# Performance work log

Hardware: AMD Instinct MI355X
Metric: run time of the kernel (lower is better)

The kernel has to match this reference:

```python
import jax, jax.numpy as jnp
import numpy as np

N_NODES = 50000
N_EDGES = 600000
IN_FEATS = 16
H_FEAT = 128
N_CLASSES = 4
N_HIDDEN_LAYERS = 19  # conv2..conv20


def setup_inputs() -> dict:
    key = jax.random.key(0)
    ks = jax.random.split(key, 10)
    x = jax.random.normal(ks[0], (N_NODES, IN_FEATS), dtype=jnp.float32)
    edge_index = jax.random.randint(ks[1], (2, N_EDGES), 0, N_NODES, dtype=jnp.int32)
    edge_attr = jax.random.uniform(ks[2], (N_EDGES, 1), dtype=jnp.float32)
    s_in = 1.0 / np.sqrt(IN_FEATS)
    s_h = 1.0 / np.sqrt(H_FEAT)
    W_in = jax.random.uniform(ks[3], (IN_FEATS, H_FEAT), minval=-s_in, maxval=s_in, dtype=jnp.float32)
    b_in = jax.random.uniform(ks[4], (H_FEAT,), minval=-s_in, maxval=s_in, dtype=jnp.float32)
    W_h = jax.random.uniform(ks[5], (N_HIDDEN_LAYERS, H_FEAT, H_FEAT), minval=-s_h, maxval=s_h, dtype=jnp.float32)
    b_h = jax.random.uniform(ks[6], (N_HIDDEN_LAYERS, H_FEAT), minval=-s_h, maxval=s_h, dtype=jnp.float32)
    W_fc = jax.random.uniform(ks[7], (H_FEAT, N_CLASSES), minval=-s_h, maxval=s_h, dtype=jnp.float32)
    b_fc = jax.random.uniform(ks[8], (N_CLASSES,), minval=-s_h, maxval=s_h, dtype=jnp.float32)
    return {"x": x, "edge_index": edge_index, "edge_attr": edge_attr,
            "W_in": W_in, "b_in": b_in, "W_h": W_h, "b_h": b_h,
            "W_fc": W_fc, "b_fc": b_fc}


def reference(x, edge_index, edge_attr, W_in, b_in, W_h, b_h, W_fc, b_fc):
    src, dst = edge_index[0], edge_index[1]
    ew = edge_attr[:, 0]  # edge_weight = edge_attr[:, 0]
    n = x.shape[0]
    # degree by dst, clamped at 1
    deg = jax.ops.segment_sum(jnp.ones(src.shape[0], dtype=x.dtype), dst, num_segments=n)
    deg_inv = 1.0 / jnp.maximum(deg, 1.0)  # [N]

    def conv(h, W, b):
        h = h @ W + b                       # [N, out]
        msg = h[src] * ew[:, None]          # [E, out]
        agg = jax.ops.segment_sum(msg, dst, num_segments=n)
        return agg * deg_inv[:, None]

    h = jax.nn.leaky_relu(conv(x, W_in, b_in))

    def step(h, params):
        W, b = params
        return jax.nn.leaky_relu(conv(h, W, b)), None

    h, _ = jax.lax.scan(step, h, (W_h, b_h))
    return h @ W_fc + b_fc  # [N, num_classes]
```

## Files before the change

### kernel.cpp

```cpp
#include <hip/hip_runtime.h>
#include <hip/hip_fp16.h>

#define N_NODES 50000
#define N_EDGES 600000
#define IN_F 16
#define HF 128
#define NC 4
#define NHL 19
#define N_FP8_LAYERS 15
#define WS_STRIDE 136

__device__ __forceinline__ float lrelu(float x) { return x > 0.f ? x : 0.01f * x; }

struct h4 { __half2 a, b; };

typedef _Float16 f16;
typedef _Float16 f16x8 __attribute__((ext_vector_type(8)));
typedef float    f32x4 __attribute__((ext_vector_type(4)));
typedef float    f32x2 __attribute__((ext_vector_type(2)));

__device__ __forceinline__ unsigned pack_fp8x4(float a, float b, float c, float d) {
    int r = __builtin_amdgcn_cvt_pk_fp8_f32(a, b, 0, false);
    r = __builtin_amdgcn_cvt_pk_fp8_f32(c, d, r, true);
    return (unsigned)r;
}


__global__ void count_deg_k(const int* __restrict__ dst, int* __restrict__ cnt) {
    int e = blockIdx.x * 256 + threadIdx.x;
    if (e < N_EDGES) atomicAdd(&cnt[dst[e]], 1);
}

__global__ void scan_k(const int* __restrict__ cnt, int* __restrict__ rowptr,
                       float* __restrict__ dinv) {
    __shared__ int wsum[16];
    __shared__ int carry_s;
    int t = threadIdx.x;
    int lane = t & 63, wid = t >> 6;
    if (t == 0) carry_s = 0;
    __syncthreads();
    for (int base = 0; base < N_NODES; base += 4096) {
        int idx = base + t * 4;
        int4 v = make_int4(0, 0, 0, 0);
        if (idx + 3 < N_NODES) v = *(const int4*)&cnt[idx];
        else {
            if (idx     < N_NODES) v.x = cnt[idx];
            if (idx + 1 < N_NODES) v.y = cnt[idx + 1];
            if (idx + 2 < N_NODES) v.z = cnt[idx + 2];
            if (idx + 3 < N_NODES) v.w = cnt[idx + 3];
        }
        if (idx + 3 < N_NODES) {
            float4 dv = make_float4(1.f / fmaxf((float)v.x, 1.f), 1.f / fmaxf((float)v.y, 1.f),
                                    1.f / fmaxf((float)v.z, 1.f), 1.f / fmaxf((float)v.w, 1.f));
            *(float4*)&dinv[idx] = dv;
        } else {
            if (idx     < N_NODES) dinv[idx]     = 1.f / fmaxf((float)v.x, 1.f);
            if (idx + 1 < N_NODES) dinv[idx + 1] = 1.f / fmaxf((float)v.y, 1.f);
            if (idx + 2 < N_NODES) dinv[idx + 2] = 1.f / fmaxf((float)v.z, 1.f);
            if (idx + 3 < N_NODES) dinv[idx + 3] = 1.f / fmaxf((float)v.w, 1.f);
        }
        int s1 = v.x + v.y, s2 = s1 + v.z, total = s2 + v.w;
        int sc = total;
#pragma unroll
        for (int off = 1; off < 64; off <<= 1) {
            int u = __shfl_up(sc, off, 64);
            if (lane >= off) sc += u;
        }
        if (lane == 63) wsum[wid] = sc;
        __syncthreads();
        if (t < 16) {
            int w = wsum[t];
#pragma unroll
            for (int off = 1; off < 16; off <<= 1) {
                int u = __shfl_up(w, off, 64);
                if (t >= off) w += u;
            }
            wsum[t] = w;
        }
        __syncthreads();
        int prefix = carry_s + (wid > 0 ? wsum[wid - 1] : 0) + (sc - total);
        if (idx     < N_NODES) rowptr[idx]     = prefix;
        if (idx + 1 < N_NODES) rowptr[idx + 1] = prefix + v.x;
        if (idx + 2 < N_NODES) rowptr[idx + 2] = prefix + s1;
        if (idx + 3 < N_NODES) rowptr[idx + 3] = prefix + s2;
        __syncthreads();
        if (t == 0) carry_s += wsum[15];
        __syncthreads();
    }
    if (t == 0) rowptr[N_NODES] = carry_s;
}

__global__ void fill_k(const int* __restrict__ src, const int* __restrict__ dst,
                       const float* __restrict__ ea, const int* __restrict__ rowptr,
                       int* __restrict__ fill, int2* __restrict__ edg,
                       const float* __restrict__ dinv) {
    int e = blockIdx.x * 256 + threadIdx.x;
    if (e < N_EDGES) {
        int d = dst[e];
        int pos = rowptr[d] + atomicAdd(&fill[d], 1);
        edg[pos] = make_int2(src[e], __float_as_int(ea[e] * dinv[d]));
    }
}


__global__ void wconv_k(const float* __restrict__ Wh, __half* __restrict__ Wt) {
    int idx = blockIdx.x * 256 + threadIdx.x;
    if (idx >= NHL * HF * HF) return;
    int l = idx / (HF * HF);
    int r = idx - l * (HF * HF);
    int n = r >> 7;
    int k = r & 127;
    Wt[idx] = __float2half(Wh[(size_t)l * HF * HF + k * HF + n]);
}


__global__ void gemm_in_k(const float* __restrict__ X, const float* __restrict__ W,
                          const float* __restrict__ b, unsigned* __restrict__ T8) {
    __shared__ float Ws[IN_F * HF];
    int t = threadIdx.x;
    ((float4*)Ws)[t]       = ((const float4*)W)[t];
    ((float4*)Ws)[t + 256] = ((const float4*)W)[t + 256];
    __syncthreads();
    int row = blockIdx.x * 16 + (t >> 4);
    if (row >= N_NODES) return;
    int tx = t & 15;
    int c0 = tx * 4, c1 = 64 + tx * 4;
    float4 a0 = *(const float4*)&b[c0];
    float4 a1 = *(const float4*)&b[c1];
    const float4* xr = (const float4*)(X + row * IN_F);
#pragma unroll
    for (int k4 = 0; k4 < 4; k4++) {
        float4 xv = xr[k4];
        const float* xp = (const float*)&xv;
#pragma unroll
        for (int kk = 0; kk < 4; kk++) {
            int k = k4 * 4 + kk;
            float4 w0 = *(const float4*)&Ws[k * HF + c0];
            float4 w1 = *(const float4*)&Ws[k * HF + c1];
            float xs = xp[kk];
            a0.x = fmaf(xs, w0.x, a0.x); a0.y = fmaf(xs, w0.y, a0.y);
            a0.z = fmaf(xs, w0.z, a0.z); a0.w = fmaf(xs, w0.w, a0.w);
            a1.x = fmaf(xs, w1.x, a1.x); a1.y = fmaf(xs, w1.y, a1.y);
            a1.z = fmaf(xs, w1.z, a1.z); a1.w = fmaf(xs, w1.w, a1.w);
        }
    }
    T8[(size_t)row * 32 + tx]      = pack_fp8x4(a0.x, a0.y, a0.z, a0.w);
    T8[(size_t)row * 32 + 16 + tx] = pack_fp8x4(a1.x, a1.y, a1.z, a1.w);
}


template <bool FP8IN, bool FP8OUT>
__global__ __launch_bounds__(256) void gemm_mfma_k(const void* __restrict__ Hin,
                                                   const __half* __restrict__ Wt,
                                                   const float* __restrict__ b,
                                                   void* __restrict__ Tout) {
    __shared__ __half Ws[HF * WS_STRIDE];
    __shared__ __half Hs[64 * WS_STRIDE];
    int t = threadIdx.x;
    int rbase = blockIdx.x * 64;
    int u16 = t & 15;
    int rg  = t >> 4;

#pragma unroll
    for (int p = 0; p < 8; p++) {
        int n = p * 16 + rg;
        *(float4*)&Ws[n * WS_STRIDE + u16 * 8] = *(const float4*)&Wt[(size_t)n * HF + u16 * 8];
    }
#pragma unroll
    for (int p = 0; p < 4; p++) {
        int rl = p * 16 + rg;
        int row = rbase + rl;
        if (row >= N_NODES) row = N_NODES - 1;
        if (FP8IN) {
            uint2 hv8 = *(const uint2*)&((const unsigned char*)Hin)[(size_t)row * HF + u16 * 8];
            f32x2 a0 = __builtin_amdgcn_cvt_pk_f32_fp8((int)hv8.x, false);
            f32x2 a1 = __builtin_amdgcn_cvt_pk_f32_fp8((int)hv8.x, true);
            f32x2 a2 = __builtin_amdgcn_cvt_pk_f32_fp8((int)hv8.y, false);
            f32x2 a3 = __builtin_amdgcn_cvt_pk_f32_fp8((int)hv8.y, true);
            h4 o0, o1;
            o0.a = __floats2half2_rn(a0.x, a0.y); o0.b = __floats2half2_rn(a1.x, a1.y);
            o1.a = __floats2half2_rn(a2.x, a2.y); o1.b = __floats2half2_rn(a3.x, a3.y);
            float4 pk;
            ((h4*)&pk)[0] = o0;
            *(h4*)((char*)&pk + 8) = o1;
            *(float4*)&Hs[rl * WS_STRIDE + u16 * 8] = pk;
        } else {
            *(float4*)&Hs[rl * WS_STRIDE + u16 * 8] =
                *(const float4*)&((const __half*)Hin)[(size_t)row * HF + u16 * 8];
        }
    }
    __syncthreads();

    int lane = t & 63;
    int w    = t >> 6;
    int wr   = w * 16;
    int m16  = lane & 15;
    int q    = lane >> 4;

    f16x8 af[4];
#pragma unroll
    for (int kc = 0; kc < 4; kc++)
        af[kc] = *(const f16x8*)&Hs[(wr + m16) * WS_STRIDE + kc * 32 + q * 8];

    f32x4 acc[8];
#pragma unroll
    for (int nt = 0; nt < 8; nt++) {
        float bv = b[nt * 16 + m16];
        acc[nt] = (f32x4){bv, bv, bv, bv};
#pragma unroll
        for (int kc = 0; kc < 4; kc++) {
            f16x8 bf = *(const f16x8*)&Ws[(nt * 16 + m16) * WS_STRIDE + kc * 32 + q * 8];
            acc[nt] = __builtin_amdgcn_mfma_f32_16x16x32_f16(af[kc], bf, acc[nt], 0, 0, 0);
        }
    }
    __syncthreads();

#pragma unroll
    for (int nt = 0; nt < 8; nt++)
#pragma unroll
        for (int r = 0; r < 4; r++)
            Hs[(wr + q * 4 + r) * WS_STRIDE + nt * 16 + m16] = __float2half(acc[nt][r]);
    __syncthreads();

#pragma unroll
    for (int p = 0; p < 4; p++) {
        int rl = p * 16 + rg;
        int row = rbase + rl;
        if (row < N_NODES) {
            float4 cv = *(float4*)&Hs[rl * WS_STRIDE + u16 * 8];
            if (FP8OUT) {
                __half2* hp = (__half2*)&cv;
                float2 f0 = __half22float2(hp[0]);
                float2 f1 = __half22float2(hp[1]);
                float2 f2 = __half22float2(hp[2]);
                float2 f3 = __half22float2(hp[3]);
                uint2 o;
                o.x = pack_fp8x4(f0.x, f0.y, f1.x, f1.y);
                o.y = pack_fp8x4(f2.x, f2.y, f3.x, f3.y);
                *(uint2*)&((unsigned char*)Tout)[(size_t)row * HF + u16 * 8] = o;
            } else {
                *(float4*)&((__half*)Tout)[(size_t)row * HF + u16 * 8] = cv;
            }
        }
    }
}


template <bool FP8IN, bool FP8OUT>
__global__ __launch_bounds__(256) void agg2_k(const void* __restrict__ Tin,
                                              void* __restrict__ O,
                                              const int* __restrict__ rowptr,
                                              const int2* __restrict__ edg) {
    int gw = blockIdx.x * 4 + (threadIdx.x >> 6);
    int vA = gw * 2;
    if (vA >= N_NODES) return;
    int lane = threadIdx.x & 63;
    int half = lane >> 5;
    int li   = lane & 31;

    int rA = __builtin_amdgcn_readfirstlane(rowptr[vA]);
    int rM = __builtin_amdgcn_readfirstlane(rowptr[vA + 1]);
    int rB = __builtin_amdgcn_readfirstlane(rowptr[vA + 2]);
    int eBase = half ? rM : rA;
    int eEnd  = half ? rB : rM;
    int degmax = max(rM - rA, rB - rM);
    int nb = (degmax + 15) >> 4;

    const h4*       T16 = (const h4*)Tin;
    const unsigned* T8  = (const unsigned*)Tin;

    float4 acc = make_float4(0.f, 0.f, 0.f, 0.f);

    for (int eb = 0; eb < nb; eb++) {
        int idx = eBase + eb * 16 + (li & 15);
        bool ok = idx < eEnd;
        int2 rec = edg[ok ? idx : 0];
        int   s_l = rec.x;
        float w_l = ok ? __int_as_float(rec.y) : 0.f;
        int sb = half << 5;
#pragma unroll
        for (int g = 0; g < 2; g++) {
            int   ss[8];
            float ww[8];
#pragma unroll
            for (int u = 0; u < 8; u++) {
                int sl = sb + g * 8 + u;
                ss[u] = __shfl(s_l, sl, 64);
                ww[u] = __shfl(w_l, sl, 64);
            }
            if (FP8IN) {
                unsigned gv[8];
#pragma unroll
                for (int u = 0; u < 8; u++)
                    gv[u] = T8[(size_t)ss[u] * 32 + li];
#pragma unroll
                for (int u = 0; u < 8; u++) {
                    f32x2 lo = __builtin_amdgcn_cvt_pk_f32_fp8((int)gv[u], false);
                    f32x2 hi = __builtin_amdgcn_cvt_pk_f32_fp8((int)gv[u], true);
                    acc.x = fmaf(lo.x, ww[u], acc.x);
                    acc.y = fmaf(lo.y, ww[u], acc.y);
                    acc.z = fmaf(hi.x, ww[u], acc.z);
                    acc.w = fmaf(hi.y, ww[u], acc.w);
                }
            } else {
                h4 hv[8];
#pragma unroll
                for (int u = 0; u < 8; u++)
                    hv[u] = T16[(size_t)ss[u] * (HF / 4) + li];
#pragma unroll
                for (int u = 0; u < 8; u++) {
                    float2 p0 = __half22float2(hv[u].a);
                    float2 p1 = __half22float2(hv[u].b);
                    acc.x = fmaf(p0.x, ww[u], acc.x);
                    acc.y = fmaf(p0.y, ww[u], acc.y);
                    acc.z = fmaf(p1.x, ww[u], acc.z);
                    acc.w = fmaf(p1.y, ww[u], acc.w);
                }
            }
        }
    }
    int v = vA + half;
    if (FP8OUT) {
        ((unsigned*)O)[(size_t)v * 32 + li] =
            pack_fp8x4(lrelu(acc.x), lrelu(acc.y), lrelu(acc.z), lrelu(acc.w));
    } else {
        h4 o;
        o.a = __floats2half2_rn(lrelu(acc.x), lrelu(acc.y));
        o.b = __floats2half2_rn(lrelu(acc.z), lrelu(acc.w));
        ((h4*)O)[(size_t)v * (HF / 4) + li] = o;
    }
}


__global__ void fc_k(const __half* __restrict__ H, const float* __restrict__ W,
                     const float* __restrict__ b, float* __restrict__ out) {
    int r = blockIdx.x * 256 + threadIdx.x;
    if (r >= N_NODES) return;
    float4 acc = *(const float4*)b;
    const h4* hp = (const h4*)(H + (size_t)r * HF);
    const float4* w4 = (const float4*)W;
#pragma unroll
    for (int k4 = 0; k4 < 32; k4++) {
        h4 hh = hp[k4];
        float2 p0 = __half22float2(hh.a);
        float2 p1 = __half22float2(hh.b);
        float4 wa = w4[k4 * 4 + 0], wb = w4[k4 * 4 + 1];
        float4 wc = w4[k4 * 4 + 2], wd = w4[k4 * 4 + 3];
        acc.x = fmaf(p0.x, wa.x, acc.x); acc.y = fmaf(p0.x, wa.y, acc.y);
        acc.z = fmaf(p0.x, wa.z, acc.z); acc.w = fmaf(p0.x, wa.w, acc.w);
        acc.x = fmaf(p0.y, wb.x, acc.x); acc.y = fmaf(p0.y, wb.y, acc.y);
        acc.z = fmaf(p0.y, wb.z, acc.z); acc.w = fmaf(p0.y, wb.w, acc.w);
        acc.x = fmaf(p1.x, wc.x, acc.x); acc.y = fmaf(p1.x, wc.y, acc.y);
        acc.z = fmaf(p1.x, wc.z, acc.z); acc.w = fmaf(p1.x, wc.w, acc.w);
        acc.x = fmaf(p1.y, wd.x, acc.x); acc.y = fmaf(p1.y, wd.y, acc.y);
        acc.z = fmaf(p1.y, wd.z, acc.z); acc.w = fmaf(p1.y, wd.w, acc.w);
    }
    *(float4*)&out[r * NC] = acc;
}


extern "C" void kernel_launch(void* const* d_in, const int* in_sizes, int n_in,
                              void* d_out, int out_size, void* d_ws, size_t ws_size,
                              hipStream_t stream) {
    const float* X   = (const float*)d_in[0];
    const int*   EI  = (const int*)d_in[1];
    const float* EA  = (const float*)d_in[2];
    const float* Win = (const float*)d_in[3];
    const float* bin = (const float*)d_in[4];
    const float* Wh  = (const float*)d_in[5];
    const float* bh  = (const float*)d_in[6];
    const float* Wfc = (const float*)d_in[7];
    const float* bfc = (const float*)d_in[8];
    float* out = (float*)d_out;
    const int* src = EI;
    const int* dst = EI + N_EDGES;

    char* ws = (char*)d_ws;
    size_t off = 0;
    void*   O   = (void*)(ws + off);   off += (size_t)N_NODES * HF * 2;
    void*   T   = (void*)(ws + off);   off += (size_t)N_NODES * HF * 2;
    __half* Wt  = (__half*)(ws + off); off += (size_t)NHL * HF * HF * 2;
    int2* edg   = (int2*)(ws + off);  off += (size_t)N_EDGES * 8;
    int* rowptr = (int*)(ws + off);   off += (((size_t)(N_NODES + 1) * 4 + 15) / 16) * 16;
    int* cnt    = (int*)(ws + off);   off += (size_t)N_NODES * 4;
    int* fill   = (int*)(ws + off);   off += (size_t)N_NODES * 4;
    float* dinv = (float*)(ws + off); off += (size_t)N_NODES * 4;

    hipMemsetAsync(cnt, 0, N_NODES * 4, stream);
    hipMemsetAsync(fill, 0, N_NODES * 4, stream);
    count_deg_k<<<(N_EDGES + 255) / 256, 256, 0, stream>>>(dst, cnt);
    scan_k<<<1, 1024, 0, stream>>>(cnt, rowptr, dinv);
    fill_k<<<(N_EDGES + 255) / 256, 256, 0, stream>>>(src, dst, EA, rowptr, fill, edg, dinv);
    wconv_k<<<(NHL * HF * HF + 255) / 256, 256, 0, stream>>>(Wh, Wt);

    const int aggg  = (N_NODES / 2 + 3) / 4;
    const int gemmg = (N_NODES + 63) / 64;

    gemm_in_k<<<(N_NODES + 15) / 16, 256, 0, stream>>>(X, Win, bin, (unsigned*)T);
    agg2_k<true, true><<<aggg, 256, 0, stream>>>(T, O, rowptr, edg);
    for (int l = 0; l < N_FP8_LAYERS; l++) {
        gemm_mfma_k<true, true><<<gemmg, 256, 0, stream>>>(
            O, Wt + (size_t)l * HF * HF, bh + (size_t)l * HF, T);
        if (l < N_FP8_LAYERS - 1)
            agg2_k<true, true><<<aggg, 256, 0, stream>>>(T, O, rowptr, edg);
        else
            agg2_k<true, false><<<aggg, 256, 0, stream>>>(T, O, rowptr, edg);
    }
    for (int l = N_FP8_LAYERS; l < NHL; l++) {
        gemm_mfma_k<false, false><<<gemmg, 256, 0, stream>>>(
            O, Wt + (size_t)l * HF * HF, bh + (size_t)l * HF, T);
        agg2_k<false, false><<<aggg, 256, 0, stream>>>(T, O, rowptr, edg);
    }
    fc_k<<<(N_NODES + 255) / 256, 256, 0, stream>>>((const __half*)O, Wfc, bfc, out);
}
```

Measured before the change: 715.8 us.

## Aggregate four nodes per wavefront with wider gathers and more FP8 layers

The aggregation kernel now has each 64-lane wavefront handle four destination nodes, with 16 lanes per node. Each lane gathers 8 features at a time (uint2 for FP8, uint4 for FP16) instead of 4, which widens memory transactions and gives more work per lane. Row pointers are loaded in a single vector load and broadcast with shuffles. The number of FP8-precision layers is also raised from 15 to 17, which cuts gather bytes further but risks accuracy loss.

```diff
diff --git a/kernel.cpp b/kernel.cpp
--- a/kernel.cpp
+++ b/kernel.cpp
@@ -7,7 +7,7 @@
 #define HF 128
 #define NC 4
 #define NHL 19
-#define N_FP8_LAYERS 15
+#define N_FP8_LAYERS 17
 #define WS_STRIDE 136
 
 __device__ __forceinline__ float lrelu(float x) { return x > 0.f ? x : 0.01f * x; }
@@ -247,37 +247,36 @@
 
 
 template <bool FP8IN, bool FP8OUT>
-__global__ __launch_bounds__(256) void agg2_k(const void* __restrict__ Tin,
+__global__ __launch_bounds__(256) void agg4_k(const void* __restrict__ Tin,
                                               void* __restrict__ O,
                                               const int* __restrict__ rowptr,
                                               const int2* __restrict__ edg) {
     int gw = blockIdx.x * 4 + (threadIdx.x >> 6);
-    int vA = gw * 2;
-    if (vA >= N_NODES) return;
+    int v0 = gw * 4;
+    if (v0 >= N_NODES) return;
     int lane = threadIdx.x & 63;
-    int half = lane >> 5;
-    int li   = lane & 31;
-
-    int rA = __builtin_amdgcn_readfirstlane(rowptr[vA]);
-    int rM = __builtin_amdgcn_readfirstlane(rowptr[vA + 1]);
-    int rB = __builtin_amdgcn_readfirstlane(rowptr[vA + 2]);
-    int eBase = half ? rM : rA;
-    int eEnd  = half ? rB : rM;
-    int degmax = max(rM - rA, rB - rM);
+    int q  = lane >> 4;
+    int li = lane & 15;
+
+    int rp = rowptr[v0 + min(lane, 4)];
+    int r0 = __shfl(rp, 0, 64), r1 = __shfl(rp, 1, 64), r2 = __shfl(rp, 2, 64);
+    int r3 = __shfl(rp, 3, 64), r4 = __shfl(rp, 4, 64);
+    int e0 = __shfl(rp, q, 64);
+    int e1 = __shfl(rp, q + 1, 64);
+    int degmax = max(max(r1 - r0, r2 - r1), max(r3 - r2, r4 - r3));
     int nb = (degmax + 15) >> 4;
 
-    const h4*       T16 = (const h4*)Tin;
-    const unsigned* T8  = (const unsigned*)Tin;
-
-    float4 acc = make_float4(0.f, 0.f, 0.f, 0.f);
+    const uint2* T8  = (const uint2*)Tin;
+    const uint4* T16 = (const uint4*)Tin;
+
+    float acc[8] = {0.f, 0.f, 0.f, 0.f, 0.f, 0.f, 0.f, 0.f};
 
     for (int eb = 0; eb < nb; eb++) {
-        int idx = eBase + eb * 16 + (li & 15);
-        bool ok = idx < eEnd;
+        int idx = e0 + eb * 16 + li;
+        bool ok = idx < e1;
         int2 rec = edg[ok ? idx : 0];
-        int   s_l = rec.x;
-        float w_l = ok ? __int_as_float(rec.y) : 0.f;
-        int sb = half << 5;
+        if (!ok) rec.y = 0;
+        int sb = q << 4;
 #pragma unroll
         for (int g = 0; g < 2; g++) {
             int   ss[8];
@@ -285,49 +284,69 @@
 #pragma unroll
             for (int u = 0; u < 8; u++) {
                 int sl = sb + g * 8 + u;
-                ss[u] = __shfl(s_l, sl, 64);
-                ww[u] = __shfl(w_l, sl, 64);
+                ss[u] = __shfl(rec.x, sl, 64);
+                ww[u] = __int_as_float(__shfl(rec.y, sl, 64));
             }
             if (FP8IN) {
-                unsigned gv[8];
+                uint2 gv[8];
 #pragma unroll
                 for (int u = 0; u < 8; u++)
-                    gv[u] = T8[(size_t)ss[u] * 32 + li];
+                    gv[u] = T8[(size_t)ss[u] * 16 + li];
 #pragma unroll
                 for (int u = 0; u < 8; u++) {
-                    f32x2 lo = __builtin_amdgcn_cvt_pk_f32_fp8((int)gv[u], false);
-                    f32x2 hi = __builtin_amdgcn_cvt_pk_f32_fp8((int)gv[u], true);
-                    acc.x = fmaf(lo.x, ww[u], acc.x);
-                    acc.y = fmaf(lo.y, ww[u], acc.y);
-                    acc.z = fmaf(hi.x, ww[u], acc.z);
-                    acc.w = fmaf(hi.y, ww[u], acc.w);
+                    f32x2 p0 = __builtin_amdgcn_cvt_pk_f32_fp8((int)gv[u].x, false);
+                    f32x2 p1 = __builtin_amdgcn_cvt_pk_f32_fp8((int)gv[u].x, true);
+                    f32x2 p2 = __builtin_amdgcn_cvt_pk_f32_fp8((int)gv[u].y, false);
+                    f32x2 p3 = __builtin_amdgcn_cvt_pk_f32_fp8((int)gv[u].y, true);
+                    acc[0] = fmaf(p0.x, ww[u], acc[0]);
+                    acc[1] = fmaf(p0.y, ww[u], acc[1]);
+                    acc[2] = fmaf(p1.x, ww[u], acc[2]);
+                    acc[3] = fmaf(p1.y, ww[u], acc[3]);
+                    acc[4] = fmaf(p2.x, ww[u], acc[4]);
+                    acc[5] = fmaf(p2.y, ww[u], acc[5]);
+                    acc[6] = fmaf(p3.x, ww[u], acc[6]);
+                    acc[7] = fmaf(p3.y, ww[u], acc[7]);
                 }
             } else {
-                h4 hv[8];
+                uint4 gv[8];
 #pragma unroll
                 for (int u = 0; u < 8; u++)
-                    hv[u] = T16[(size_t)ss[u] * (HF / 4) + li];
+                    gv[u] = T16[(size_t)ss[u] * 16 + li];
 #pragma unroll
                 for (int u = 0; u < 8; u++) {
-                    float2 p0 = __half22float2(hv[u].a);
-                    float2 p1 = __half22float2(hv[u].b);
-                    acc.x = fmaf(p0.x, ww[u], acc.x);
-                    acc.y = fmaf(p0.y, ww[u], acc.y);
-                    acc.z = fmaf(p1.x, ww[u], acc.z);
-                    acc.w = fmaf(p1.y, ww[u], acc.w);
+                    __half2* hp = (__half2*)&gv[u];
+                    float2 p0 = __half22float2(hp[0]);
+                    float2 p1 = __half22float2(hp[1]);
+                    float2 p2 = __half22float2(hp[2]);
+                    float2 p3 = __half22float2(hp[3]);
+                    acc[0] = fmaf(p0.x, ww[u], acc[0]);
+                    acc[1] = fmaf(p0.y, ww[u], acc[1]);
+                    acc[2] = fmaf(p1.x, ww[u], acc[2]);
+                    acc[3] = fmaf(p1.y, ww[u], acc[3]);
+                    acc[4] = fmaf(p2.x, ww[u], acc[4]);
+                    acc[5] = fmaf(p2.y, ww[u], acc[5]);
+                    acc[6] = fmaf(p3.x, ww[u], acc[6]);
+                    acc[7] = fmaf(p3.y, ww[u], acc[7]);
                 }
             }
         }
     }
-    int v = vA + half;
+    int v = v0 + q;
     if (FP8OUT) {
-        ((unsigned*)O)[(size_t)v * 32 + li] =
-            pack_fp8x4(lrelu(acc.x), lrelu(acc.y), lrelu(acc.z), lrelu(acc.w));
+        uint2 o;
+        o.x = pack_fp8x4(lrelu(acc[0]), lrelu(acc[1]), lrelu(acc[2]), lrelu(acc[3]));
+        o.y = pack_fp8x4(lrelu(acc[4]), lrelu(acc[5]), lrelu(acc[6]), lrelu(acc[7]));
+        ((uint2*)O)[(size_t)v * 16 + li] = o;
     } else {
-        h4 o;
-        o.a = __floats2half2_rn(lrelu(acc.x), lrelu(acc.y));
-        o.b = __floats2half2_rn(lrelu(acc.z), lrelu(acc.w));
-        ((h4*)O)[(size_t)v * (HF / 4) + li] = o;
+        h4 oa, ob;
+        oa.a = __floats2half2_rn(lrelu(acc[0]), lrelu(acc[1]));
+        oa.b = __floats2half2_rn(lrelu(acc[2]), lrelu(acc[3]));
+        ob.a = __floats2half2_rn(lrelu(acc[4]), lrelu(acc[5]));
+        ob.b = __floats2half2_rn(lrelu(acc[6]), lrelu(acc[7]));
+        uint4 ov;
+        ((h4*)&ov)[0] = oa;
+        *(h4*)((char*)&ov + 8) = ob;
+        ((uint4*)O)[(size_t)v * 16 + li] = ov;
     }
 }
 
@@ -393,23 +412,23 @@
     fill_k<<<(N_EDGES + 255) / 256, 256, 0, stream>>>(src, dst, EA, rowptr, fill, edg, dinv);
     wconv_k<<<(NHL * HF * HF + 255) / 256, 256, 0, stream>>>(Wh, Wt);
 
-    const int aggg  = (N_NODES / 2 + 3) / 4;
+    const int aggg  = (N_NODES / 4 + 3) / 4;
     const int gemmg = (N_NODES + 63) / 64;
 
     gemm_in_k<<<(N_NODES + 15) / 16, 256, 0, stream>>>(X, Win, bin, (unsigned*)T);
-    agg2_k<true, true><<<aggg, 256, 0, stream>>>(T, O, rowptr, edg);
+    agg4_k<true, true><<<aggg, 256, 0, stream>>>(T, O, rowptr, edg);
     for (int l = 0; l < N_FP8_LAYERS; l++) {
         gemm_mfma_k<true, true><<<gemmg, 256, 0, stream>>>(
             O, Wt + (size_t)l * HF * HF, bh + (size_t)l * HF, T);
         if (l < N_FP8_LAYERS - 1)
-            agg2_k<true, true><<<aggg, 256, 0, stream>>>(T, O, rowptr, edg);
+            agg4_k<true, true><<<aggg, 256, 0, stream>>>(T, O, rowptr, edg);
         else
-            agg2_k<true, false><<<aggg, 256, 0, stream>>>(T, O, rowptr, edg);
+            agg4_k<true, false><<<aggg, 256, 0, stream>>>(T, O, rowptr, edg);
     }
     for (int l = N_FP8_LAYERS; l < NHL; l++) {
         gemm_mfma_k<false, false><<<gemmg, 256, 0, stream>>>(
             O, Wt + (size_t)l * HF * HF, bh + (size_t)l * HF, T);
-        agg2_k<false, false><<<aggg, 256, 0, stream>>>(T, O, rowptr, edg);
+        agg4_k<false, false><<<aggg, 256, 0, stream>>>(T, O, rowptr, edg);
     }
     fc_k<<<(N_NODES + 255) / 256, 256, 0, stream>>>((const __half*)O, Wfc, bfc, out);
 }
```

After: 705.7 us. About the same (-1.4%).
